# Kernel optimization log

Measured on AMD Instinct MI355X. Metric: run time of the kernel, lower is better.

The kernel has to match this reference:

```python
import jax, jax.numpy as jnp
import numpy as np

ATOM_FEA = 128
NBR_FEA = 64
NUM_NBR = 12
N_NODES = 50000
N_EDGES = N_NODES * NUM_NBR
BN_EPS = 1e-5


def setup_inputs() -> dict:
    key = jax.random.key(0)
    ks = jax.random.split(key, 8)
    x = jax.random.normal(ks[0], (N_NODES, ATOM_FEA), dtype=jnp.float32)
    # CGCNN layout: each node has exactly NUM_NBR edges, contiguous by source node
    src = jnp.repeat(jnp.arange(N_NODES, dtype=jnp.int64), NUM_NBR)
    nbr = jax.random.randint(ks[1], (N_EDGES,), 0, N_NODES, dtype=jnp.int64)
    edge_index = jnp.stack([src, nbr], axis=0)
    edge_attr = jax.random.normal(ks[2], (N_EDGES, NBR_FEA), dtype=jnp.float32)
    in_dim = 2 * ATOM_FEA + NBR_FEA
    out_dim = 2 * ATOM_FEA
    lim = 1.0 / np.sqrt(in_dim)
    W = jax.random.uniform(ks[3], (out_dim, in_dim), jnp.float32, -lim, lim)
    b = jax.random.uniform(ks[4], (out_dim,), jnp.float32, -lim, lim)
    bn1_g = jnp.ones((out_dim,), jnp.float32)
    bn1_b = jnp.zeros((out_dim,), jnp.float32)
    bn2_g = jnp.ones((ATOM_FEA,), jnp.float32)
    bn2_b = jnp.zeros((ATOM_FEA,), jnp.float32)
    return {"x": x, "edge_index": edge_index, "edge_attr": edge_attr,
            "W": W, "b": b, "bn1_g": bn1_g, "bn1_b": bn1_b,
            "bn2_g": bn2_g, "bn2_b": bn2_b}


def _batchnorm(h, gamma, beta):
    # training-mode BN: biased batch variance, eps=1e-5 (torch default)
    mean = jnp.mean(h, axis=0)
    var = jnp.var(h, axis=0)
    return (h - mean) * jax.lax.rsqrt(var + BN_EPS) * gamma + beta


def reference(x, edge_index, edge_attr, W, b, bn1_g, bn1_b, bn2_g, bn2_b):
    n_nodes, fea = x.shape
    num_nbr = edge_index.shape[1] // n_nodes
    # gather + concat: [E, 2F + nbr_fea]
    total = jnp.concatenate([x[edge_index[1]], x[edge_index[0]], edge_attr], axis=1)
    gated = total @ W.T + b                      # [E, 2F]
    gated = _batchnorm(gated, bn1_g, bn1_b)
    nbr_filter, nbr_core = jnp.split(gated, 2, axis=1)
    msg = jax.nn.sigmoid(nbr_filter) * jax.nn.softplus(nbr_core)  # [E, F]
    nbr_sumed = msg.reshape(n_nodes, num_nbr, fea).sum(axis=1)    # [N, F]
    nbr_sumed = _batchnorm(nbr_sumed, bn2_g, bn2_b)
    return jax.nn.softplus(x + nbr_sumed)
```

## Files before the change

kernel.cpp:

```cpp
#include <hip/hip_runtime.h>
#include <math.h>

#define ATOM_FEA 128
#define NBR_FEA  64
#define IN_DIM   320
#define OUT_DIM  256

#define M_TILE   48
#define GRID_G   1792
#define GRID_3   2048
#define RB1      32

typedef float  f32x4 __attribute__((ext_vector_type(4)));
typedef short  s16x8 __attribute__((ext_vector_type(8)));

__device__ __forceinline__ float softplusf(float v) {
    float e = __expf(-fabsf(v));
    return fmaxf(v, 0.f) + __logf(1.f + e);
}
__device__ __forceinline__ float sigmoidf(float v) {
    return __builtin_amdgcn_rcpf(1.f + __expf(-v));
}
__device__ __forceinline__ float bf2f(unsigned short h) {
    return __uint_as_float(((unsigned)h) << 16);
}
__device__ __forceinline__ unsigned pk2(float a, float b) {
    unsigned r;
    asm("v_cvt_pk_bf16_f32 %0, %1, %2" : "=v"(r) : "v"(a), "v"(b));
    return r;
}

__global__ __launch_bounds__(256) void k1_mfma(
    const float* __restrict__ x, const float* __restrict__ W,
    const float* __restrict__ bvec,
    unsigned short* __restrict__ Abf, unsigned short* __restrict__ Bbf,
    int nNodes)
{
    __shared__ alignas(16) char sx[64 * 272];
    const int tid  = threadIdx.x;
    const int wave = tid >> 6;
    const int lane = tid & 63;
    const int li   = lane & 15;
    const int quad = lane >> 4;
    const int cTile = blockIdx.x * 64;
    const int nTile = blockIdx.y * 64;
    const int cOff  = (cTile < 256) ? cTile : (cTile - 256);
    const int kBase = (cTile < 256) ? 0 : 128;
    unsigned short* dst = (cTile < 256) ? Abf : Bbf;

    s16x8 bf[4][4];
    #pragma unroll
    for (int ks = 0; ks < 4; ++ks)
        #pragma unroll
        for (int ns = 0; ns < 4; ++ns) {
            const float* wr = W + (size_t)(cOff + ns * 16 + li) * IN_DIM + kBase + ks * 32 + quad * 8;
            float4 va = *(const float4*)wr;
            float4 vb = *(const float4*)(wr + 4);
            union { uint4 u; s16x8 v; } cv;
            cv.u = make_uint4(pk2(va.x, va.y), pk2(va.z, va.w),
                              pk2(vb.x, vb.y), pk2(vb.z, vb.w));
            bf[ks][ns] = cv.v;
        }

    #pragma unroll
    for (int i = 0; i < 8; ++i) {
        int idx = tid + i * 256;
        int r = idx >> 5, q = idx & 31;
        int gn = nTile + r;
        float4 v = make_float4(0.f, 0.f, 0.f, 0.f);
        if (gn < nNodes) v = *(const float4*)(x + (size_t)gn * ATOM_FEA + q * 4);
        uint2 u; u.x = pk2(v.x, v.y); u.y = pk2(v.z, v.w);
        *(uint2*)(sx + r * 272 + q * 8) = u;
    }
    __syncthreads();

    s16x8 af[4];
    #pragma unroll
    for (int ks = 0; ks < 4; ++ks)
        af[ks] = *(const s16x8*)(sx + (wave * 16 + li) * 272 + (ks * 32 + quad * 8) * 2);

    f32x4 acc[4] = {};
    #pragma unroll
    for (int ks = 0; ks < 4; ++ks)
        #pragma unroll
        for (int ns = 0; ns < 4; ++ns)
            acc[ns] = __builtin_amdgcn_mfma_f32_16x16x32_bf16(bf[ks][ns], af[ks], acc[ns], 0, 0, 0);

    const int node = nTile + wave * 16 + li;
    if (node < nNodes) {
        #pragma unroll
        for (int ns = 0; ns < 4; ++ns) {
            const int c0 = cOff + ns * 16 + quad * 4;
            float4 bb = make_float4(0.f, 0.f, 0.f, 0.f);
            if (kBase) bb = *(const float4*)(bvec + c0);
            uint2 o;
            o.x = pk2(acc[ns][0] + bb.x, acc[ns][1] + bb.y);
            o.y = pk2(acc[ns][2] + bb.z, acc[ns][3] + bb.w);
            *(uint2*)(dst + (size_t)node * 256 + c0) = o;
        }
    }
}

__global__ __launch_bounds__(256) void k2_fused(
    const unsigned short* __restrict__ Abf, const unsigned short* __restrict__ Bbf,
    const float* __restrict__ ea, const int* __restrict__ ei,
    const float* __restrict__ W,
    unsigned short* __restrict__ gated, float* __restrict__ part,
    int nEdges)
{
    const int tid  = threadIdx.x;
    const int wave = tid >> 6;
    const int lane = tid & 63;
    const int li   = lane & 15;
    const int quad = lane >> 4;

    s16x8 bfr[2][4];
    #pragma unroll
    for (int ks = 0; ks < 2; ++ks)
        #pragma unroll
        for (int ns = 0; ns < 4; ++ns) {
            int chn = wave * 64 + ns * 16 + li;
            const float* wr = W + (size_t)chn * IN_DIM + 256 + ks * 32 + quad * 8;
            float4 va = *(const float4*)wr;
            float4 vb = *(const float4*)(wr + 4);
            union { uint4 u; s16x8 v; } cv;
            cv.u = make_uint4(pk2(va.x, va.y), pk2(va.z, va.w),
                              pk2(vb.x, vb.y), pk2(vb.z, vb.w));
            bfr[ks][ns] = cv.v;
        }

    int noff[3];
    #pragma unroll
    for (int ms = 0; ms < 3; ++ms) noff[ms] = (int)((unsigned)(ms * 16 + li) / 12u);

    const int cB = wave * 64 + quad * 4;

    f32x4 s4[4]  = {};
    f32x4 s24[4] = {};

    const int nTiles = (nEdges + M_TILE - 1) / M_TILE;
    for (int t = blockIdx.x; t < nTiles; t += gridDim.x) {
        const int tBase = t * M_TILE;

        int nb[3];
        #pragma unroll
        for (int ms = 0; ms < 3; ++ms) {
            int e = tBase + ms * 16 + li;
            nb[ms] = (e < nEdges) ? ei[nEdges + e] : 0;
        }

        #pragma unroll
        for (int ms = 0; ms < 3; ++ms) {
            const int e    = tBase + ms * 16 + li;
            const bool ok  = (e < nEdges);
            const int node = t * 4 + noff[ms];

            uint2 a2[4], b2[4];
            if (ok) {
                #pragma unroll
                for (int ns = 0; ns < 4; ++ns) {
                    const int c0 = cB + ns * 16;
                    a2[ns] = *(const uint2*)(Abf + (size_t)nb[ms] * 256 + c0);
                    b2[ns] = *(const uint2*)(Bbf + (size_t)node * 256 + c0);
                }
            }

            s16x8 af[2];
            #pragma unroll
            for (int ks = 0; ks < 2; ++ks) {
                float4 va = make_float4(0.f, 0.f, 0.f, 0.f);
                float4 vb = make_float4(0.f, 0.f, 0.f, 0.f);
                if (ok) {
                    const float* er = ea + (size_t)e * NBR_FEA + ks * 32 + quad * 8;
                    va = *(const float4*)er;
                    vb = *(const float4*)(er + 4);
                }
                union { uint4 u; s16x8 v; } cv;
                cv.u = make_uint4(pk2(va.x, va.y), pk2(va.z, va.w),
                                  pk2(vb.x, vb.y), pk2(vb.z, vb.w));
                af[ks] = cv.v;
            }

            f32x4 acc[4] = {};
            #pragma unroll
            for (int ks = 0; ks < 2; ++ks)
                #pragma unroll
                for (int ns = 0; ns < 4; ++ns)
                    acc[ns] = __builtin_amdgcn_mfma_f32_16x16x32_bf16(
                        bfr[ks][ns], af[ks], acc[ns], 0, 0, 0);

            if (ok) {
                #pragma unroll
                for (int ns = 0; ns < 4; ++ns) {
                    const int c0 = cB + ns * 16;
                    float g0 = acc[ns][0] + bf2f((unsigned short)(a2[ns].x & 0xffffu))
                                          + bf2f((unsigned short)(b2[ns].x & 0xffffu));
                    float g1 = acc[ns][1] + bf2f((unsigned short)(a2[ns].x >> 16))
                                          + bf2f((unsigned short)(b2[ns].x >> 16));
                    float g2 = acc[ns][2] + bf2f((unsigned short)(a2[ns].y & 0xffffu))
                                          + bf2f((unsigned short)(b2[ns].y & 0xffffu));
                    float g3 = acc[ns][3] + bf2f((unsigned short)(a2[ns].y >> 16))
                                          + bf2f((unsigned short)(b2[ns].y >> 16));
                    s4[ns][0] += g0; s4[ns][1] += g1; s4[ns][2] += g2; s4[ns][3] += g3;
                    s24[ns][0] = fmaf(g0, g0, s24[ns][0]);
                    s24[ns][1] = fmaf(g1, g1, s24[ns][1]);
                    s24[ns][2] = fmaf(g2, g2, s24[ns][2]);
                    s24[ns][3] = fmaf(g3, g3, s24[ns][3]);
                    uint2 o; o.x = pk2(g0, g1); o.y = pk2(g2, g3);
                    *(uint2*)(gated + (size_t)e * 256 + c0) = o;
                }
            }
        }
    }

    #pragma unroll
    for (int m = 1; m < 16; m <<= 1) {
        #pragma unroll
        for (int ns = 0; ns < 4; ++ns) {
            #pragma unroll
            for (int k = 0; k < 4; ++k) {
                s4[ns][k]  += __shfl_xor(s4[ns][k],  m);
                s24[ns][k] += __shfl_xor(s24[ns][k], m);
            }
        }
    }
    if (li == 0) {
        #pragma unroll
        for (int ns = 0; ns < 4; ++ns) {
            const int c0 = cB + ns * 16;
            *(f32x4*)(part + (size_t)blockIdx.x * 512 + c0)       = s4[ns];
            *(f32x4*)(part + (size_t)blockIdx.x * 512 + 256 + c0) = s24[ns];
        }
    }
}

__global__ __launch_bounds__(512) void k2b1(
    const float* __restrict__ part, float* __restrict__ out, int nRows, int rowsPerBlk)
{
    const int c = threadIdx.x;
    int r0 = blockIdx.x * rowsPerBlk;
    int r1 = min(r0 + rowsPerBlk, nRows);
    float s = 0.f;
    for (int r = r0; r < r1; ++r) s += part[(size_t)r * 512 + c];
    out[(size_t)blockIdx.x * 512 + c] = s;
}
__global__ __launch_bounds__(256) void k2b2(
    const float* __restrict__ p1, const float* __restrict__ g1v,
    const float* __restrict__ b1v, float* __restrict__ stats, float invE)
{
    const int c = threadIdx.x;
    float s = 0.f, s2 = 0.f;
    for (int r = 0; r < RB1; ++r) {
        s  += p1[(size_t)r * 512 + c];
        s2 += p1[(size_t)r * 512 + 256 + c];
    }
    float mean = s * invE;
    float var = fmaf(-mean, mean, s2 * invE);
    float sc = g1v[c] * rsqrtf(var + 1e-5f);
    stats[c] = sc;
    stats[256 + c] = fmaf(-mean, sc, b1v[c]);
}

__global__ __launch_bounds__(256) void k3_msg2(
    const unsigned short* __restrict__ gated, const float* __restrict__ stats,
    float* __restrict__ NS, float* __restrict__ part2, int nNodes)
{
    const int tid = threadIdx.x;
    const int o  = tid & 15;
    const int nl = tid >> 4;
    float scF[8], shF[8], scC[8], shC[8];
    #pragma unroll
    for (int k = 0; k < 8; ++k) {
        int cf = o * 8 + k;
        scF[k] = stats[cf];        shF[k] = stats[256 + cf];
        scC[k] = stats[128 + cf];  shC[k] = stats[384 + cf];
    }
    float sA[8] = {}, s2A[8] = {};
    for (int n = blockIdx.x * 16 + nl; n < nNodes; n += gridDim.x * 16) {
        float m[8] = {};
        for (int j = 0; j < 12; ++j) {
            size_t base = (size_t)(n * 12 + j) * 256;
            uint4 uf = *(const uint4*)(gated + base + o * 8);
            uint4 uc = *(const uint4*)(gated + base + 128 + o * 8);
            unsigned fu[4] = {uf.x, uf.y, uf.z, uf.w};
            unsigned cu[4] = {uc.x, uc.y, uc.z, uc.w};
            #pragma unroll
            for (int q = 0; q < 4; ++q) {
                float f0 = fmaf(bf2f((unsigned short)(fu[q] & 0xffffu)), scF[q*2],   shF[q*2]);
                float f1 = fmaf(bf2f((unsigned short)(fu[q] >> 16)),     scF[q*2+1], shF[q*2+1]);
                float c0 = fmaf(bf2f((unsigned short)(cu[q] & 0xffffu)), scC[q*2],   shC[q*2]);
                float c1 = fmaf(bf2f((unsigned short)(cu[q] >> 16)),     scC[q*2+1], shC[q*2+1]);
                m[q*2]   = fmaf(sigmoidf(f0), softplusf(c0), m[q*2]);
                m[q*2+1] = fmaf(sigmoidf(f1), softplusf(c1), m[q*2+1]);
            }
        }
        float4 o0 = {m[0], m[1], m[2], m[3]};
        float4 o1 = {m[4], m[5], m[6], m[7]};
        *(float4*)(NS + (size_t)n * 128 + o * 8)     = o0;
        *(float4*)(NS + (size_t)n * 128 + o * 8 + 4) = o1;
        #pragma unroll
        for (int k = 0; k < 8; ++k) {
            sA[k] += m[k];
            s2A[k] = fmaf(m[k], m[k], s2A[k]);
        }
    }
    __shared__ float red[2][16][128];
    #pragma unroll
    for (int k = 0; k < 8; ++k) {
        red[0][nl][o * 8 + k] = sA[k];
        red[1][nl][o * 8 + k] = s2A[k];
    }
    __syncthreads();
    if (tid < 128) {
        float s = 0.f, s2 = 0.f;
        #pragma unroll
        for (int r = 0; r < 16; ++r) {
            s  += red[0][r][tid];
            s2 += red[1][r][tid];
        }
        part2[(size_t)blockIdx.x * 256 + tid]       = s;
        part2[(size_t)blockIdx.x * 256 + 128 + tid] = s2;
    }
}

__global__ __launch_bounds__(256) void k3b1(
    const float* __restrict__ part2, float* __restrict__ out, int nRows, int rowsPerBlk)
{
    const int c = threadIdx.x;
    int r0 = blockIdx.x * rowsPerBlk;
    int r1 = min(r0 + rowsPerBlk, nRows);
    float s = 0.f;
    for (int r = r0; r < r1; ++r) s += part2[(size_t)r * 256 + c];
    out[(size_t)blockIdx.x * 256 + c] = s;
}
__global__ __launch_bounds__(128) void k3b2(
    const float* __restrict__ p1, const float* __restrict__ g2v,
    const float* __restrict__ b2v, float* __restrict__ stats2, float invN)
{
    const int c = threadIdx.x;
    float s = 0.f, s2 = 0.f;
    for (int r = 0; r < RB1; ++r) {
        s  += p1[(size_t)r * 256 + c];
        s2 += p1[(size_t)r * 256 + 128 + c];
    }
    float mean = s * invN;
    float var = fmaf(-mean, mean, s2 * invN);
    float sc = g2v[c] * rsqrtf(var + 1e-5f);
    stats2[c] = sc;
    stats2[128 + c] = fmaf(-mean, sc, b2v[c]);
}

__global__ __launch_bounds__(256) void k4_final(
    const float* __restrict__ x, const float* __restrict__ ns,
    const float* __restrict__ stats2, float* __restrict__ out, int total4)
{
    int idx = blockIdx.x * 256 + threadIdx.x;
    for (int i = idx; i < total4; i += gridDim.x * 256) {
        int cq = i & 31;
        float4 xv = ((const float4*)x)[i];
        float4 sv = ((const float4*)ns)[i];
        float4 sc = ((const float4*)stats2)[cq];
        float4 sh = ((const float4*)(stats2 + 128))[cq];
        float4 o;
        o.x = softplusf(fmaf(sv.x, sc.x, sh.x) + xv.x);
        o.y = softplusf(fmaf(sv.y, sc.y, sh.y) + xv.y);
        o.z = softplusf(fmaf(sv.z, sc.z, sh.z) + xv.z);
        o.w = softplusf(fmaf(sv.w, sc.w, sh.w) + xv.w);
        ((float4*)out)[i] = o;
    }
}

extern "C" void kernel_launch(void* const* d_in, const int* in_sizes, int n_in,
                              void* d_out, int out_size, void* d_ws, size_t ws_size,
                              hipStream_t stream)
{
    const float* x   = (const float*)d_in[0];
    const int*   ei  = (const int*)d_in[1];
    const float* ea  = (const float*)d_in[2];
    const float* W   = (const float*)d_in[3];
    const float* b   = (const float*)d_in[4];
    const float* g1v = (const float*)d_in[5];
    const float* b1v = (const float*)d_in[6];
    const float* g2v = (const float*)d_in[7];
    const float* b2v = (const float*)d_in[8];
    float* out = (float*)d_out;

    const int nNodes = in_sizes[0] / ATOM_FEA;
    const int nEdges = in_sizes[1] / 2;

    unsigned short* Abf   = (unsigned short*)d_ws;
    unsigned short* Bbf   = Abf + (size_t)nNodes * 256;
    unsigned short* gated = Bbf + (size_t)nNodes * 256;
    float* NS  = (float*)(gated + (size_t)nEdges * 256);
    float* P1  = NS  + (size_t)nNodes * 128;
    float* P1b = P1  + (size_t)GRID_G * 512;
    float* P2  = P1b + (size_t)RB1 * 512;
    float* P2b = P2  + (size_t)GRID_3 * 256;
    float* S1  = P2b + (size_t)RB1 * 256;
    float* S2  = S1 + 512;
    (void)ws_size; (void)n_in; (void)out_size;

    dim3 grid1(8, (nNodes + 63) / 64);
    k1_mfma<<<grid1, 256, 0, stream>>>(x, W, b, Abf, Bbf, nNodes);

    k2_fused<<<GRID_G, 256, 0, stream>>>(Abf, Bbf, ea, ei, W, gated, P1, nEdges);
    k2b1<<<RB1, 512, 0, stream>>>(P1, P1b, GRID_G, (GRID_G + RB1 - 1) / RB1);
    k2b2<<<1, 256, 0, stream>>>(P1b, g1v, b1v, S1, 1.f / (float)nEdges);
    k3_msg2<<<GRID_3, 256, 0, stream>>>(gated, S1, NS, P2, nNodes);
    k3b1<<<RB1, 256, 0, stream>>>(P2, P2b, GRID_3, (GRID_3 + RB1 - 1) / RB1);
    k3b2<<<1, 128, 0, stream>>>(P2b, g2v, b2v, S2, 1.f / (float)nNodes);
    k4_final<<<2048, 256, 0, stream>>>(x, NS, S2, out, nNodes * 32);
}
```

Before: 713.0 us.

## Stage MFMA tile in LDS and gather neighbor rows coalesced per node

The edge-feature MFMA results for a 48-edge tile are packed to bf16 and written to shared memory. Each wave then handles one node: it gathers the 12 neighbor rows of the precomputed A projection with all 64 lanes reading contiguous 8-byte chunks, adds the node's B row, accumulates BN statistics and writes gated. This replaces scattered 8-byte gathers laid out in MFMA fragment order and needs only one B-row load per node. Per-block statistics are now reduced across waves through shared memory, and the grid shrinks to 1024 blocks. The cost is two block barriers per tile and extra LDS traffic.

New measurement: 753.7 us. 5.7% more time.

```diff
diff --git a/kernel.cpp b/kernel.cpp
--- a/kernel.cpp
+++ b/kernel.cpp
@@ -7,9 +7,12 @@
 #define OUT_DIM  256
 
 #define M_TILE   48
-#define GRID_G   1792
+#define GRID_G   1024
 #define GRID_3   2048
 #define RB1      32
+
+#define X_STR    528
+#define SMEMX    (M_TILE * X_STR)
 
 typedef float  f32x4 __attribute__((ext_vector_type(4)));
 typedef short  s16x8 __attribute__((ext_vector_type(8)));
@@ -106,8 +109,9 @@
     const float* __restrict__ ea, const int* __restrict__ ei,
     const float* __restrict__ W,
     unsigned short* __restrict__ gated, float* __restrict__ part,
-    int nEdges)
-{
+    int nNodes, int nEdges)
+{
+    __shared__ alignas(16) char smem[SMEMX];
     const int tid  = threadIdx.x;
     const int wave = tid >> 6;
     const int lane = tid & 63;
@@ -129,42 +133,28 @@
             bfr[ks][ns] = cv.v;
         }
 
-    int noff[3];
-    #pragma unroll
-    for (int ms = 0; ms < 3; ++ms) noff[ms] = (int)((unsigned)(ms * 16 + li) / 12u);
-
-    const int cB = wave * 64 + quad * 4;
-
-    f32x4 s4[4]  = {};
-    f32x4 s24[4] = {};
+    const int cB  = wave * 64 + quad * 4;
+    const int chq = lane;
+
+    f32x4 s4  = {0.f, 0.f, 0.f, 0.f};
+    f32x4 s24 = {0.f, 0.f, 0.f, 0.f};
 
     const int nTiles = (nEdges + M_TILE - 1) / M_TILE;
     for (int t = blockIdx.x; t < nTiles; t += gridDim.x) {
         const int tBase = t * M_TILE;
-
-        int nb[3];
+        const int node  = t * 4 + wave;
+        const bool okN  = (node < nNodes);
+
+        int nbj[12];
+        #pragma unroll
+        for (int j = 0; j < 12; ++j)
+            nbj[j] = okN ? ei[nEdges + node * 12 + j] : 0;
+
+        f32x4 acc[3][4] = {};
         #pragma unroll
         for (int ms = 0; ms < 3; ++ms) {
-            int e = tBase + ms * 16 + li;
-            nb[ms] = (e < nEdges) ? ei[nEdges + e] : 0;
-        }
-
-        #pragma unroll
-        for (int ms = 0; ms < 3; ++ms) {
-            const int e    = tBase + ms * 16 + li;
-            const bool ok  = (e < nEdges);
-            const int node = t * 4 + noff[ms];
-
-            uint2 a2[4], b2[4];
-            if (ok) {
-                #pragma unroll
-                for (int ns = 0; ns < 4; ++ns) {
-                    const int c0 = cB + ns * 16;
-                    a2[ns] = *(const uint2*)(Abf + (size_t)nb[ms] * 256 + c0);
-                    b2[ns] = *(const uint2*)(Bbf + (size_t)node * 256 + c0);
-                }
-            }
-
+            const int e   = tBase + ms * 16 + li;
+            const bool ok = (e < nEdges);
             s16x8 af[2];
             #pragma unroll
             for (int ks = 0; ks < 2; ++ks) {
@@ -180,57 +170,74 @@
                                   pk2(vb.x, vb.y), pk2(vb.z, vb.w));
                 af[ks] = cv.v;
             }
-
-            f32x4 acc[4] = {};
             #pragma unroll
             for (int ks = 0; ks < 2; ++ks)
                 #pragma unroll
                 for (int ns = 0; ns < 4; ++ns)
-                    acc[ns] = __builtin_amdgcn_mfma_f32_16x16x32_bf16(
-                        bfr[ks][ns], af[ks], acc[ns], 0, 0, 0);
-
-            if (ok) {
-                #pragma unroll
-                for (int ns = 0; ns < 4; ++ns) {
-                    const int c0 = cB + ns * 16;
-                    float g0 = acc[ns][0] + bf2f((unsigned short)(a2[ns].x & 0xffffu))
-                                          + bf2f((unsigned short)(b2[ns].x & 0xffffu));
-                    float g1 = acc[ns][1] + bf2f((unsigned short)(a2[ns].x >> 16))
-                                          + bf2f((unsigned short)(b2[ns].x >> 16));
-                    float g2 = acc[ns][2] + bf2f((unsigned short)(a2[ns].y & 0xffffu))
-                                          + bf2f((unsigned short)(b2[ns].y & 0xffffu));
-                    float g3 = acc[ns][3] + bf2f((unsigned short)(a2[ns].y >> 16))
-                                          + bf2f((unsigned short)(b2[ns].y >> 16));
-                    s4[ns][0] += g0; s4[ns][1] += g1; s4[ns][2] += g2; s4[ns][3] += g3;
-                    s24[ns][0] = fmaf(g0, g0, s24[ns][0]);
-                    s24[ns][1] = fmaf(g1, g1, s24[ns][1]);
-                    s24[ns][2] = fmaf(g2, g2, s24[ns][2]);
-                    s24[ns][3] = fmaf(g3, g3, s24[ns][3]);
-                    uint2 o; o.x = pk2(g0, g1); o.y = pk2(g2, g3);
-                    *(uint2*)(gated + (size_t)e * 256 + c0) = o;
-                }
+                    acc[ms][ns] = __builtin_amdgcn_mfma_f32_16x16x32_bf16(
+                        bfr[ks][ns], af[ks], acc[ms][ns], 0, 0, 0);
+        }
+
+        __syncthreads();
+
+        #pragma unroll
+        for (int ms = 0; ms < 3; ++ms)
+            #pragma unroll
+            for (int ns = 0; ns < 4; ++ns) {
+                const int row = ms * 16 + li;
+                uint2 o;
+                o.x = pk2(acc[ms][ns][0], acc[ms][ns][1]);
+                o.y = pk2(acc[ms][ns][2], acc[ms][ns][3]);
+                *(uint2*)(smem + row * X_STR + (cB + ns * 16) * 2) = o;
             }
-        }
-    }
-
-    #pragma unroll
-    for (int m = 1; m < 16; m <<= 1) {
-        #pragma unroll
-        for (int ns = 0; ns < 4; ++ns) {
-            #pragma unroll
-            for (int k = 0; k < 4; ++k) {
-                s4[ns][k]  += __shfl_xor(s4[ns][k],  m);
-                s24[ns][k] += __shfl_xor(s24[ns][k], m);
+
+        __syncthreads();
+
+        if (okN) {
+            uint2 bn2 = *(const uint2*)(Bbf + (size_t)node * 256 + chq * 4);
+            const float Bn0 = bf2f((unsigned short)(bn2.x & 0xffffu));
+            const float Bn1 = bf2f((unsigned short)(bn2.x >> 16));
+            const float Bn2 = bf2f((unsigned short)(bn2.y & 0xffffu));
+            const float Bn3 = bf2f((unsigned short)(bn2.y >> 16));
+
+            uint2 a2[12];
+            #pragma unroll
+            for (int j = 0; j < 12; ++j)
+                a2[j] = *(const uint2*)(Abf + (size_t)nbj[j] * 256 + chq * 4);
+
+            #pragma unroll
+            for (int j = 0; j < 12; ++j) {
+                const int e = node * 12 + j;
+                uint2 xv = *(const uint2*)(smem + (wave * 12 + j) * X_STR + chq * 8);
+                float g0 = bf2f((unsigned short)(xv.x & 0xffffu)) + bf2f((unsigned short)(a2[j].x & 0xffffu)) + Bn0;
+                float g1 = bf2f((unsigned short)(xv.x >> 16))     + bf2f((unsigned short)(a2[j].x >> 16))     + Bn1;
+                float g2 = bf2f((unsigned short)(xv.y & 0xffffu)) + bf2f((unsigned short)(a2[j].y & 0xffffu)) + Bn2;
+                float g3 = bf2f((unsigned short)(xv.y >> 16))     + bf2f((unsigned short)(a2[j].y >> 16))     + Bn3;
+                s4[0] += g0; s4[1] += g1; s4[2] += g2; s4[3] += g3;
+                s24[0] = fmaf(g0, g0, s24[0]); s24[1] = fmaf(g1, g1, s24[1]);
+                s24[2] = fmaf(g2, g2, s24[2]); s24[3] = fmaf(g3, g3, s24[3]);
+                uint2 o; o.x = pk2(g0, g1); o.y = pk2(g2, g3);
+                *(uint2*)(gated + (size_t)e * 256 + chq * 4) = o;
             }
         }
     }
-    if (li == 0) {
-        #pragma unroll
-        for (int ns = 0; ns < 4; ++ns) {
-            const int c0 = cB + ns * 16;
-            *(f32x4*)(part + (size_t)blockIdx.x * 512 + c0)       = s4[ns];
-            *(f32x4*)(part + (size_t)blockIdx.x * 512 + 256 + c0) = s24[ns];
-        }
+
+    __syncthreads();
+    float* red = (float*)smem;
+    *(f32x4*)(red + (size_t)(wave * 64 + chq) * 8)     = s4;
+    *(f32x4*)(red + (size_t)(wave * 64 + chq) * 8 + 4) = s24;
+    __syncthreads();
+    {
+        const int c = tid;
+        const int g = c >> 2, k = c & 3;
+        float s = 0.f, s2 = 0.f;
+        #pragma unroll
+        for (int w = 0; w < 4; ++w) {
+            s  += red[(w * 64 + g) * 8 + k];
+            s2 += red[(w * 64 + g) * 8 + 4 + k];
+        }
+        part[(size_t)blockIdx.x * 512 + c]       = s;
+        part[(size_t)blockIdx.x * 512 + 256 + c] = s2;
     }
 }
 
@@ -403,7 +410,7 @@
     dim3 grid1(8, (nNodes + 63) / 64);
     k1_mfma<<<grid1, 256, 0, stream>>>(x, W, b, Abf, Bbf, nNodes);
 
-    k2_fused<<<GRID_G, 256, 0, stream>>>(Abf, Bbf, ea, ei, W, gated, P1, nEdges);
+    k2_fused<<<GRID_G, 256, 0, stream>>>(Abf, Bbf, ea, ei, W, gated, P1, nNodes, nEdges);
     k2b1<<<RB1, 512, 0, stream>>>(P1, P1b, GRID_G, (GRID_G + RB1 - 1) / RB1);
     k2b2<<<1, 256, 0, stream>>>(P1b, g1v, b1v, S1, 1.f / (float)nEdges);
     k3_msg2<<<GRID_3, 256, 0, stream>>>(gated, S1, NS, P2, nNodes);
```
